# Kernel optimization log

Measured on AMD Instinct MI355X. Metric: run time of the kernel, lower is better.

## Reference

```python
import jax, jax.numpy as jnp
import numpy as np

N, IN_C, HID, OUT_C, DEPTH = 4096, 128, 256, 128, 3
KS = [2048, 1024, 512]  # ceil(0.5 * N_level)
E = 131072


def glorot(key, fan_in, fan_out):
    lim = np.sqrt(6.0 / (fan_in + fan_out))
    return jax.random.uniform(key, (fan_in, fan_out), jnp.float32, -lim, lim)


def build_adj(edge_index, n):
    # symmetric, self-loop-free adjacency with unit edge weights
    A = jnp.zeros((n, n), jnp.float32)
    A = A.at[edge_index[0], edge_index[1]].set(1.0)
    A = jnp.maximum(A, A.T)
    return A * (1.0 - jnp.eye(n, dtype=jnp.float32))


def gcn(x, A, W, b):
    # GCNConv(improved=True): A_hat = A + 2I, symmetric normalization
    n = A.shape[0]
    Ah = A + 2.0 * jnp.eye(n, dtype=A.dtype)
    deg = Ah.sum(axis=1)
    dinv = jnp.where(deg > 0, deg ** -0.5, 0.0)
    An = dinv[:, None] * Ah * dinv[None, :]
    return An @ (x @ W) + b


def augment(A):
    # remove self loops, add self loops (w=1), square (spspmm), remove self loops
    n = A.shape[0]
    I = jnp.eye(n, dtype=A.dtype)
    Al = A * (1.0 - I) + I
    A2 = Al @ Al
    return A2 * (1.0 - I)


def topk_pool(x, A, p, k):
    score = jnp.tanh((x @ p) / jnp.linalg.norm(p))
    vals, perm = jax.lax.top_k(score, k)
    return x[perm] * vals[:, None], A[perm][:, perm], perm


def setup_inputs() -> dict:
    key = jax.random.key(0)
    ks = jax.random.split(key, 16)
    x = jax.random.normal(ks[0], (N, IN_C), jnp.float32)
    edge_index = jax.random.randint(ks[1], (2, E), 0, N, jnp.int32)
    d = {"x": x, "edge_index": edge_index}
    d["Wd0"], d["bd0"] = glorot(ks[2], IN_C, HID), jnp.zeros((HID,), jnp.float32)
    d["Wd1"], d["bd1"] = glorot(ks[3], HID, HID), jnp.zeros((HID,), jnp.float32)
    d["Wd2"], d["bd2"] = glorot(ks[4], HID, HID), jnp.zeros((HID,), jnp.float32)
    d["Wd3"], d["bd3"] = glorot(ks[5], HID, HID), jnp.zeros((HID,), jnp.float32)
    d["p1"] = jax.random.normal(ks[6], (HID,), jnp.float32)
    d["p2"] = jax.random.normal(ks[7], (HID,), jnp.float32)
    d["p3"] = jax.random.normal(ks[8], (HID,), jnp.float32)
    d["Wu0"], d["bu0"] = glorot(ks[9], HID, HID), jnp.zeros((HID,), jnp.float32)
    d["Wu1"], d["bu1"] = glorot(ks[10], HID, HID), jnp.zeros((HID,), jnp.float32)
    d["Wu2"], d["bu2"] = glorot(ks[11], HID, OUT_C), jnp.zeros((OUT_C,), jnp.float32)
    return d


def reference(x, edge_index, Wd0, bd0, Wd1, bd1, Wd2, bd2, Wd3, bd3,
              p1, p2, p3, Wu0, bu0, Wu1, bu1, Wu2, bu2):
    n = x.shape[0]
    A = build_adj(edge_index, n)
    x = jax.nn.relu(gcn(x, A, Wd0, bd0))
    xs, As, perms = [x], [A], []
    down = [(Wd1, bd1), (Wd2, bd2), (Wd3, bd3)]
    pools = [p1, p2, p3]
    for i in range(DEPTH):
        A = augment(A)
        x, A, perm = topk_pool(x, A, pools[i], KS[i])
        x = jax.nn.relu(gcn(x, A, *down[i]))
        if i < DEPTH - 1:
            xs.append(x)
            As.append(A)
        perms.append(perm)
    up = [(Wu0, bu0), (Wu1, bu1), (Wu2, bu2)]
    for i in range(DEPTH):
        j = DEPTH - 1 - i
        res, perm = xs[j], perms[j]
        u = jnp.zeros_like(res).at[perm].set(x)
        x = res + u  # sum_res=True
        x = gcn(x, As[j], *up[i])
        if i < DEPTH - 1:
            x = jax.nn.relu(x)
    return x
```

## Files before the change

kernel.cpp:

```cpp
#include <hip/hip_runtime.h>


typedef __attribute__((ext_vector_type(8))) short bf16x8;
typedef __attribute__((ext_vector_type(4))) short s16x4;
typedef __attribute__((ext_vector_type(4))) float f32x4;

__device__ __forceinline__ short f2bf(float f) {
    unsigned u = __builtin_bit_cast(unsigned, f);
    u += 0x7FFFu + ((u >> 16) & 1u);
    return (short)(u >> 16);
}
__device__ __forceinline__ float bf2f(short s) {
    unsigned u = ((unsigned)(unsigned short)s) << 16;
    return __builtin_bit_cast(float, u);
}

#define GLL16(gsrc, ldst)                                                        \
    __builtin_amdgcn_global_load_lds(                                            \
        (__attribute__((address_space(1))) void*)(gsrc),                         \
        (__attribute__((address_space(3))) void*)(ldst), 16, 0, 0)

template<int MODE, int EPI>
__global__ __launch_bounds__(256, 2)
void gemm_bt(const short* __restrict__ Ah, const short* __restrict__ Al,
             const short* __restrict__ Bh, const short* __restrict__ Bl,
             float* __restrict__ Cf, int M, int N, int K, int kChunk)
{
    if (EPI == 1 && (int)blockIdx.y > (int)blockIdx.x) return;

    __shared__ short sAh[128 * 32];
    __shared__ short sBh[128 * 32];
    __shared__ short sAl[(MODE == 2) ? 128 * 32 : 8];
    __shared__ short sBl[(MODE >= 1) ? 128 * 32 : 8];

    const int t    = threadIdx.x;
    const int lane = t & 63;
    const int wave = t >> 6;
    const int tM   = blockIdx.y * 128;
    const int tN   = blockIdx.x * 128;
    const int k0   = blockIdx.z * kChunk;

    const int wm  = (wave >> 1) * 64;
    const int wn  = (wave & 1) * 64;
    const int l15 = lane & 15;
    const int g8  = (lane >> 4) * 8;

    f32x4 acc[4][4];
    const f32x4 zero = {0.f, 0.f, 0.f, 0.f};
#pragma unroll
    for (int i = 0; i < 4; i++)
#pragma unroll
        for (int j = 0; j < 4; j++) acc[i][j] = zero;

    const int i0 = t, i1 = t + 256;
    const short* a0 = Ah + (size_t)(tM + (i0 >> 2)) * K + (i0 & 3) * 8;
    const short* a1 = Ah + (size_t)(tM + (i1 >> 2)) * K + (i1 & 3) * 8;
    const short* b0 = Bh + (size_t)(tN + (i0 >> 2)) * K + (i0 & 3) * 8;
    const short* b1 = Bh + (size_t)(tN + (i1 >> 2)) * K + (i1 & 3) * 8;
    const short *bl0 = nullptr, *bl1 = nullptr, *al0 = nullptr, *al1 = nullptr;
    if (MODE >= 1) {
        bl0 = Bl + (size_t)(tN + (i0 >> 2)) * K + (i0 & 3) * 8;
        bl1 = Bl + (size_t)(tN + (i1 >> 2)) * K + (i1 & 3) * 8;
    }
    if (MODE == 2) {
        al0 = Al + (size_t)(tM + (i0 >> 2)) * K + (i0 & 3) * 8;
        al1 = Al + (size_t)(tM + (i1 >> 2)) * K + (i1 & 3) * 8;
    }

    for (int kb = k0; kb < k0 + kChunk; kb += 32) {
        GLL16(a0 + kb, &sAh[i0 * 8]);
        GLL16(a1 + kb, &sAh[i1 * 8]);
        GLL16(b0 + kb, &sBh[i0 * 8]);
        GLL16(b1 + kb, &sBh[i1 * 8]);
        if (MODE >= 1) { GLL16(bl0 + kb, &sBl[i0 * 8]); GLL16(bl1 + kb, &sBl[i1 * 8]); }
        if (MODE == 2) { GLL16(al0 + kb, &sAl[i0 * 8]); GLL16(al1 + kb, &sAl[i1 * 8]); }
        __syncthreads();

        bf16x8 aF[4], bF[4], aL[4], bL[4];
#pragma unroll
        for (int i = 0; i < 4; i++)
            aF[i] = *(const bf16x8*)&sAh[(wm + i * 16 + l15) * 32 + g8];
#pragma unroll
        for (int j = 0; j < 4; j++)
            bF[j] = *(const bf16x8*)&sBh[(wn + j * 16 + l15) * 32 + g8];
        if (MODE >= 1)
#pragma unroll
            for (int j = 0; j < 4; j++)
                bL[j] = *(const bf16x8*)&sBl[(wn + j * 16 + l15) * 32 + g8];
        if (MODE == 2)
#pragma unroll
            for (int i = 0; i < 4; i++)
                aL[i] = *(const bf16x8*)&sAl[(wm + i * 16 + l15) * 32 + g8];

#pragma unroll
        for (int i = 0; i < 4; i++)
#pragma unroll
            for (int j = 0; j < 4; j++) {
                acc[i][j] = __builtin_amdgcn_mfma_f32_16x16x32_bf16(aF[i], bF[j], acc[i][j], 0, 0, 0);
                if (MODE >= 1)
                    acc[i][j] = __builtin_amdgcn_mfma_f32_16x16x32_bf16(aF[i], bL[j], acc[i][j], 0, 0, 0);
                if (MODE == 2)
                    acc[i][j] = __builtin_amdgcn_mfma_f32_16x16x32_bf16(aL[i], bF[j], acc[i][j], 0, 0, 0);
            }
        __syncthreads();
    }

    const int r4 = (lane >> 4) * 4;
    if (EPI == 3) {
        float* CT = Cf + (size_t)blockIdx.z * M * N;
#pragma unroll
        for (int i = 0; i < 4; i++)
#pragma unroll
            for (int j = 0; j < 4; j++) {
                const int col   = tN + wn + j * 16 + l15;
                const int rbase = tM + wm + i * 16 + r4;
                *(f32x4*)&CT[(size_t)col * M + rbase] = acc[i][j];
            }
    } else {
        float* Cg = Cf + (size_t)blockIdx.z * M * N;
#pragma unroll
        for (int i = 0; i < 4; i++)
#pragma unroll
            for (int j = 0; j < 4; j++) {
                const int col = tN + wn + j * 16 + l15;
                float* cp = Cg + (size_t)(tM + wm + i * 16 + r4) * N + col;
#pragma unroll
                for (int r = 0; r < 4; r++) cp[(size_t)r * N] = acc[i][j][r];
            }
        if (EPI == 1 && tM != tN) {
#pragma unroll
            for (int i = 0; i < 4; i++)
#pragma unroll
                for (int j = 0; j < 4; j++) {
                    const int col   = tN + wn + j * 16 + l15;
                    const int rbase = tM + wm + i * 16 + r4;
                    *(f32x4*)&Cg[(size_t)col * N + rbase] = acc[i][j];
                }
        }
    }
}


__global__ void prep(const float* __restrict__ Wd0, const float* __restrict__ Wd1,
                     const float* __restrict__ Wd2, const float* __restrict__ Wd3,
                     const float* __restrict__ Wu0, const float* __restrict__ Wu1,
                     const float* __restrict__ Wu2, const float* __restrict__ x0,
                     short* __restrict__ Wth, short* __restrict__ Wtl,
                     short* __restrict__ Xh, short* __restrict__ Xl,
                     unsigned long long* __restrict__ M0)
{
    int t = blockIdx.x * 256 + threadIdx.x;
    float v; int dst;
    if (t < 32768)       { int e = t;          v = Wd0[e]; dst = 0      + (e & 255) * 128 + (e >> 8); }
    else if (t < 98304)  { int e = t - 32768;  v = Wd1[e]; dst = 32768  + (e & 255) * 256 + (e >> 8); }
    else if (t < 163840) { int e = t - 98304;  v = Wd2[e]; dst = 98304  + (e & 255) * 256 + (e >> 8); }
    else if (t < 229376) { int e = t - 163840; v = Wd3[e]; dst = 163840 + (e & 255) * 256 + (e >> 8); }
    else if (t < 294912) { int e = t - 229376; v = Wu0[e]; dst = 229376 + (e & 255) * 256 + (e >> 8); }
    else if (t < 360448) { int e = t - 294912; v = Wu1[e]; dst = 294912 + (e & 255) * 256 + (e >> 8); }
    else if (t < 393216) { int e = t - 360448; v = Wu2[e]; dst = 360448 + (e & 127) * 256 + (e >> 7); }
    else if (t < 917504) {
        int e = t - 393216;
        v = x0[e];
        short h = f2bf(v);
        Xh[e] = h; Xl[e] = f2bf(v - bf2f(h));
        return;
    } else {
        M0[t - 917504] = 0ull;
        return;
    }
    short h = f2bf(v);
    Wth[dst] = h; Wtl[dst] = f2bf(v - bf2f(h));
}

__global__ void build_bits(const int* __restrict__ ei, int E,
                           unsigned long long* __restrict__ M0)
{
    int e = blockIdx.x * 256 + threadIdx.x;
    if (e >= E) return;
    int i = ei[e], j = ei[E + e];
    if (i != j) {
        atomicOr(&M0[(size_t)i * 64 + (j >> 6)], 1ull << (j & 63));
        atomicOr(&M0[(size_t)j * 64 + (i >> 6)], 1ull << (i & 63));
    }
}

__global__ void row_compact_bits(const unsigned long long* __restrict__ M0,
                                 int* __restrict__ csr, float* __restrict__ rs)
{
    int row = blockIdx.x * 4 + (threadIdx.x >> 6);
    int lane = threadIdx.x & 63;
    unsigned long long w = M0[(size_t)row * 64 + lane];
    int c = __popcll(w);
    int incl = c;
    for (int off = 1; off < 64; off <<= 1) {
        int v = __shfl_up(incl, off);
        if (lane >= off) incl += v;
    }
    int base = incl - c;
    int* out = csr + (size_t)row * 128;
    while (w) {
        int b = __ffsll((unsigned long long)w) - 1;
        if (base < 128) out[base] = lane * 64 + b;
        base++;
        w &= w - 1;
    }
    if (lane == 63) rs[row] = (float)incl;
}

__global__ void mask_gather(const unsigned long long* __restrict__ M0,
                            const int* __restrict__ perm,
                            unsigned long long* __restrict__ mask,
                            float* __restrict__ rs, int kk)
{
    int t = blockIdx.x * 256 + threadIdx.x;
    if (t < kk) rs[t] = 0.f;
    int r = t >> 6, l = t & 63;
    int u = perm[r];
    unsigned long long w = M0[(size_t)u * 64 + l];
    if ((u >> 6) == l) w |= 1ull << (u & 63);
    mask[t] = w;
}

#define PSTR2 18
__global__ __launch_bounds__(256, 8)
void popc_aug_p(const unsigned long long* __restrict__ mask,
                short* __restrict__ Cp)
{
    const int bx = blockIdx.x, by = blockIdx.y, z = blockIdx.z;
    if (by > bx) return;
    __shared__ unsigned long long a[64 * PSTR2];
    __shared__ unsigned long long b[64 * PSTR2];
    const int t = threadIdx.x;
#pragma unroll
    for (int p = 0; p < 4; p++) {
        int idx = p * 256 + t;
        int rr = idx >> 4, w = idx & 15;
        a[rr * PSTR2 + w] = mask[((size_t)(by * 64 + rr)) * 64 + z * 16 + w];
        b[rr * PSTR2 + w] = mask[((size_t)(bx * 64 + rr)) * 64 + z * 16 + w];
    }
    __syncthreads();
    const int i0 = (t >> 4) * 4;
    const int j0 = t & 15;
    int acc[4][4];
#pragma unroll
    for (int qi = 0; qi < 4; qi++)
#pragma unroll
        for (int qj = 0; qj < 4; qj++) acc[qi][qj] = 0;
#pragma unroll
    for (int w = 0; w < 16; w += 2) {
        ulong2 av[4], bv[4];
#pragma unroll
        for (int q = 0; q < 4; q++) av[q] = *(const ulong2*)&a[(i0 + q) * PSTR2 + w];
#pragma unroll
        for (int q = 0; q < 4; q++) bv[q] = *(const ulong2*)&b[(j0 + 16 * q) * PSTR2 + w];
#pragma unroll
        for (int qi = 0; qi < 4; qi++)
#pragma unroll
            for (int qj = 0; qj < 4; qj++) {
                acc[qi][qj] += __builtin_popcountll(av[qi].x & bv[qj].x);
                acc[qi][qj] += __builtin_popcountll(av[qi].y & bv[qj].y);
            }
    }
    short* out = Cp + ((size_t)z * 1024 + (size_t)(by * 32 + bx)) * 4096;
#pragma unroll
    for (int qi = 0; qi < 4; qi++)
#pragma unroll
        for (int qj = 0; qj < 4; qj++)
            out[(i0 + qi) * 64 + j0 + 16 * qj] = (short)acc[qi][qj];
}

__global__ __launch_bounds__(256)
void aug_merge(const short* __restrict__ Cp, int kk,
               short* __restrict__ Ahs, float* __restrict__ rs)
{
    const int bx = blockIdx.x, by = blockIdx.y;
    if (by > bx) return;
    __shared__ float tile[64][65];
    __shared__ float rsum[64], csum[64];
    const int t = threadIdx.x;
    const int i  = t >> 2;
    const int c0 = (t & 3) * 16;
    const size_t tb = (size_t)(by * 32 + bx) * 4096;
    const size_t ss = (size_t)1024 * 4096;
    if (t < 64) { rsum[t] = 0.f; csum[t] = 0.f; }

    int v[16];
#pragma unroll
    for (int q = 0; q < 16; q++) v[q] = 0;
    for (int s = 0; s < 4; s++) {
        bf16x8 p0 = *(const bf16x8*)&Cp[tb + s * ss + i * 64 + c0];
        bf16x8 p1 = *(const bf16x8*)&Cp[tb + s * ss + i * 64 + c0 + 8];
#pragma unroll
        for (int q = 0; q < 8; q++) { v[q] += (int)p0[q]; v[8 + q] += (int)p1[q]; }
    }
    const int gi = by * 64 + i;
    float rp = 0.f;
    s16x4 pk[4];
#pragma unroll
    for (int q = 0; q < 16; q++) {
        const int gj = bx * 64 + c0 + q;
        float val = (gi == gj) ? 0.f : (float)v[q];
        tile[i][c0 + q] = val;
        rp += val;
        pk[q >> 2][q & 3] = f2bf(val);
    }
#pragma unroll
    for (int q = 0; q < 4; q++)
        *(s16x4*)&Ahs[(size_t)gi * kk + bx * 64 + c0 + q * 4] = pk[q];
    __syncthreads();
    atomicAdd(&rsum[i], rp);
    if (bx != by) {
        float cpv = 0.f;
#pragma unroll
        for (int q = 0; q < 16; q++) {
            float val = tile[c0 + q][i];
            cpv += val;
            pk[q >> 2][q & 3] = f2bf(val);
        }
#pragma unroll
        for (int q = 0; q < 4; q++)
            *(s16x4*)&Ahs[(size_t)(bx * 64 + i) * kk + by * 64 + c0 + q * 4] = pk[q];
        atomicAdd(&csum[i], cpv);
    }
    __syncthreads();
    if (t < 64) {
        atomicAdd(&rs[by * 64 + t], rsum[t]);
        if (bx != by) atomicAdd(&rs[bx * 64 + t], csum[t]);
    }
}

__global__ void z_reduce(const float* __restrict__ Cp, int S,
                         const float* __restrict__ rs,
                         short* __restrict__ Zh, short* __restrict__ Zl,
                         int n, int C)
{
    int t4 = (blockIdx.x * 256 + threadIdx.x) * 4;
    int r = t4 % n;
    size_t stride = (size_t)n * C;
    f32x4 v = {0.f, 0.f, 0.f, 0.f};
    for (int s = 0; s < S; s++) v += *(const f32x4*)&Cp[t4 + s * stride];
    f32x4 rsv = *(const f32x4*)&rs[r];
    s16x4 zh, zl;
#pragma unroll
    for (int q = 0; q < 4; q++) {
        float z = v[q] / sqrtf(rsv[q] + 2.f);
        short h = f2bf(z);
        zh[q] = h; zl[q] = f2bf(z - bf2f(h));
    }
    *(s16x4*)&Zh[t4] = zh;
    *(s16x4*)&Zl[t4] = zl;
}

__global__ void zf_reduce(const float* __restrict__ Cp, int S,
                          const float* __restrict__ rs,
                          float* __restrict__ Zf, int n, int C)
{
    int t4 = (blockIdx.x * 256 + threadIdx.x) * 4;
    int r = t4 / C;
    size_t stride = (size_t)n * C;
    f32x4 v = {0.f, 0.f, 0.f, 0.f};
    for (int s = 0; s < S; s++) v += *(const f32x4*)&Cp[t4 + s * stride];
    float d = 1.f / sqrtf(rs[r] + 2.f);
    v *= d;
    *(f32x4*)&Zf[t4] = v;
}

template<int CN, int RELU>
__global__ __launch_bounds__(256)
void spmm_gcn(const int* __restrict__ csr, const float* __restrict__ rs,
              const float* __restrict__ Zf, const float* __restrict__ b,
              float* __restrict__ out)
{
    const int lane = threadIdx.x & 63;
    const int row  = blockIdx.x * 4 + (threadIdx.x >> 6);
    const int dg   = (int)rs[row];
    const int* nb  = csr + (size_t)row * 128;
    if (CN == 256) {
        const int c = lane * 4;
        float4 acc = {0.f, 0.f, 0.f, 0.f};
        int q = 0;
        for (; q + 4 <= dg; q += 4) {
            int j0 = nb[q], j1 = nb[q+1], j2 = nb[q+2], j3 = nb[q+3];
            float4 z0 = *(const float4*)&Zf[(size_t)j0 * CN + c];
            float4 z1 = *(const float4*)&Zf[(size_t)j1 * CN + c];
            float4 z2 = *(const float4*)&Zf[(size_t)j2 * CN + c];
            float4 z3 = *(const float4*)&Zf[(size_t)j3 * CN + c];
            acc.x += z0.x; acc.y += z0.y; acc.z += z0.z; acc.w += z0.w;
            acc.x += z1.x; acc.y += z1.y; acc.z += z1.z; acc.w += z1.w;
            acc.x += z2.x; acc.y += z2.y; acc.z += z2.z; acc.w += z2.w;
            acc.x += z3.x; acc.y += z3.y; acc.z += z3.z; acc.w += z3.w;
        }
        for (; q < dg; q++) {
            float4 z = *(const float4*)&Zf[(size_t)nb[q] * CN + c];
            acc.x += z.x; acc.y += z.y; acc.z += z.z; acc.w += z.w;
        }
        float d = 1.f / sqrtf(rs[row] + 2.f);
        float4 zi = *(const float4*)&Zf[(size_t)row * CN + c];
        float4 bb = *(const float4*)&b[c];
        float4 g;
        g.x = d * acc.x + 2.f * d * zi.x + bb.x;
        g.y = d * acc.y + 2.f * d * zi.y + bb.y;
        g.z = d * acc.z + 2.f * d * zi.z + bb.z;
        g.w = d * acc.w + 2.f * d * zi.w + bb.w;
        if (RELU) {
            g.x = fmaxf(g.x, 0.f); g.y = fmaxf(g.y, 0.f);
            g.z = fmaxf(g.z, 0.f); g.w = fmaxf(g.w, 0.f);
        }
        *(float4*)&out[(size_t)row * CN + c] = g;
    } else {
        const int c = lane * 2;
        float2 acc = {0.f, 0.f};
        int q = 0;
        for (; q + 4 <= dg; q += 4) {
            int j0 = nb[q], j1 = nb[q+1], j2 = nb[q+2], j3 = nb[q+3];
            float2 z0 = *(const float2*)&Zf[(size_t)j0 * CN + c];
            float2 z1 = *(const float2*)&Zf[(size_t)j1 * CN + c];
            float2 z2 = *(const float2*)&Zf[(size_t)j2 * CN + c];
            float2 z3 = *(const float2*)&Zf[(size_t)j3 * CN + c];
            acc.x += z0.x; acc.y += z0.y;
            acc.x += z1.x; acc.y += z1.y;
            acc.x += z2.x; acc.y += z2.y;
            acc.x += z3.x; acc.y += z3.y;
        }
        for (; q < dg; q++) {
            float2 z = *(const float2*)&Zf[(size_t)nb[q] * CN + c];
            acc.x += z.x; acc.y += z.y;
        }
        float d = 1.f / sqrtf(rs[row] + 2.f);
        float2 zi = *(const float2*)&Zf[(size_t)row * CN + c];
        float2 g;
        g.x = d * acc.x + 2.f * d * zi.x + b[c];
        g.y = d * acc.y + 2.f * d * zi.y + b[c + 1];
        if (RELU) { g.x = fmaxf(g.x, 0.f); g.y = fmaxf(g.y, 0.f); }
        *(float2*)&out[(size_t)row * CN + c] = g;
    }
}

__global__ void gcn_final(const float* __restrict__ Cp, int S,
                          const short* __restrict__ Zh, const short* __restrict__ Zl,
                          const float* __restrict__ rs, const float* __restrict__ b,
                          float* __restrict__ out, short* __restrict__ oh,
                          short* __restrict__ ol, int k, int C, int relu,
                          const int* __restrict__ inv, const float* __restrict__ res)
{
    int t4 = (blockIdx.x * 256 + threadIdx.x) * 4;
    int j = t4 / C, c = t4 - j * C;
    int r = inv ? inv[j] : j;
    f32x4 v = res ? *(const f32x4*)&res[t4] : (f32x4){0.f, 0.f, 0.f, 0.f};
    if (r >= 0) {
        size_t base = (size_t)r * C + c;
        size_t stride = (size_t)k * C;
        f32x4 az = {0.f, 0.f, 0.f, 0.f};
        for (int s = 0; s < S; s++) az += *(const f32x4*)&Cp[base + s * stride];
        float d = 1.f / sqrtf(rs[r] + 2.f);
        f32x4 bb = *(const f32x4*)&b[c];
#pragma unroll
        for (int q = 0; q < 4; q++) {
            size_t zi = (size_t)(c + q) * k + r;
            float zz = bf2f(Zh[zi]) + bf2f(Zl[zi]);
            float g = d * az[q] + 2.f * d * zz + bb[q];
            if (relu && g < 0.f) g = 0.f;
            v[q] += g;
        }
    }
    *(f32x4*)&out[t4] = v;
    if (oh) {
        s16x4 hh, ll;
#pragma unroll
        for (int q = 0; q < 4; q++) {
            short h = f2bf(v[q]);
            hh[q] = h; ll[q] = f2bf(v[q] - bf2f(h));
        }
        *(s16x4*)&oh[t4] = hh;
        *(s16x4*)&ol[t4] = ll;
    }
}

__global__ void score_kernel(const float* __restrict__ x,
                             const float* __restrict__ p,
                             float* __restrict__ score, int n,
                             int* __restrict__ rankb)
{
    int row = blockIdx.x * 4 + (threadIdx.x >> 6);
    int lane = threadIdx.x & 63;
    float4 pv = ((const float4*)p)[lane];
    float4 xv = ((const float4*)(x + (size_t)row * 256))[lane];
    double nn  = (double)pv.x * pv.x + (double)pv.y * pv.y +
                 (double)pv.z * pv.z + (double)pv.w * pv.w;
    double acc = (double)xv.x * pv.x + (double)xv.y * pv.y +
                 (double)xv.z * pv.z + (double)xv.w * pv.w;
    for (int off = 32; off; off >>= 1) {
        acc += __shfl_down(acc, off);
        nn  += __shfl_down(nn, off);
    }
    if (lane == 0) {
        score[row] = tanhf((float)(acc / sqrt(nn)));
        rankb[row] = 0;
    }
}

__device__ __forceinline__ unsigned long long packkey(float s, int i) {
    unsigned u = __builtin_bit_cast(unsigned, s);
    u = (u & 0x80000000u) ? ~u : (u | 0x80000000u);
    return ((unsigned long long)u << 32) | (unsigned)(0xFFFFFFFFu - (unsigned)i);
}

__global__ __launch_bounds__(256)
void rank_count(const float* __restrict__ score,
                int* __restrict__ rankb)
{
    __shared__ unsigned long long sk[256];
    int i = blockIdx.x * 256 + threadIdx.x;
    int j = blockIdx.y * 256 + threadIdx.x;
    sk[threadIdx.x] = packkey(score[j], j);
    unsigned long long mykey = packkey(score[i], i);
    __syncthreads();
    int part = 0;
#pragma unroll 16
    for (int q = 0; q < 256; q++) part += (sk[q] > mykey) ? 1 : 0;
    atomicAdd(&rankb[i], part);
}

__global__ void rank_final(const float* __restrict__ score,
                           const int* __restrict__ rankb, int k,
                           int* __restrict__ perm, float* __restrict__ vals,
                           int* __restrict__ inv)
{
    int i = blockIdx.x * 256 + threadIdx.x;
    int rank = rankb[i];
    if (rank < k) { perm[rank] = i; vals[rank] = score[i]; }
    inv[i] = (rank < k) ? rank : -1;
}

__global__ void gather_x_hl(const float* __restrict__ xold,
                            const int* __restrict__ perm,
                            const float* __restrict__ vals,
                            short* __restrict__ Xh, short* __restrict__ Xl, int C)
{
    int t4 = (blockIdx.x * 256 + threadIdx.x) * 4;
    int r = t4 / C, c = t4 - r * C;
    float vv = vals[r];
    f32x4 x = *(const f32x4*)&xold[(size_t)perm[r] * C + c];
    s16x4 hh, ll;
#pragma unroll
    for (int q = 0; q < 4; q++) {
        float v = x[q] * vv;
        short h = f2bf(v);
        hh[q] = h; ll[q] = f2bf(v - bf2f(h));
    }
    *(s16x4*)&Xh[t4] = hh;
    *(s16x4*)&Xl[t4] = ll;
}

__global__ void gatherG_h(const short* __restrict__ A, int n,
                          const int* __restrict__ perm,
                          short* __restrict__ Gh, int kk,
                          float* __restrict__ rsz)
{
    int idx = blockIdx.x * 256 + threadIdx.x;
    if (idx < kk) rsz[idx] = 0.f;
    int t8 = idx * 8;
    if (t8 >= kk * n) return;
    int r = t8 / n, c0 = t8 - r * n;
    int pr = perm[r];
    bf16x8 a = *(const bf16x8*)&A[(size_t)pr * n + c0];
    if (pr >= c0 && pr < c0 + 8)
        a[pr - c0] = f2bf(bf2f(a[pr - c0]) + 1.f);
    *(bf16x8*)&Gh[t8] = a;
}

__global__ void gatherG_hl(const short* __restrict__ Ahi, const short* __restrict__ Alo,
                           int n, const int* __restrict__ perm,
                           short* __restrict__ Gh, short* __restrict__ Gl, int kk,
                           float* __restrict__ rsz)
{
    int idx = blockIdx.x * 256 + threadIdx.x;
    if (idx < kk) rsz[idx] = 0.f;
    int t8 = idx * 8;
    if (t8 >= kk * n) return;
    int r = t8 / n, c0 = t8 - r * n;
    int pr = perm[r];
    bf16x8 ah = *(const bf16x8*)&Ahi[(size_t)pr * n + c0];
    bf16x8 al = *(const bf16x8*)&Alo[(size_t)pr * n + c0];
    bf16x8 gh, gl;
#pragma unroll
    for (int q = 0; q < 8; q++) {
        float v = bf2f(ah[q]) + bf2f(al[q]) + ((c0 + q == pr) ? 1.f : 0.f);
        short h = f2bf(v);
        gh[q] = h; gl[q] = f2bf(v - bf2f(h));
    }
    *(bf16x8*)&Gh[t8] = gh;
    *(bf16x8*)&Gl[t8] = gl;
}

template<bool LO>
__global__ void aug_finish_f(const float* __restrict__ Cp, int S, int kk,
                             short* __restrict__ Ahs, short* __restrict__ Als,
                             float* __restrict__ rs)
{
    int t4 = (blockIdx.x * 256 + threadIdx.x) * 4;
    int r = t4 / kk, c0 = t4 - r * kk;
    size_t stride = (size_t)kk * kk;
    f32x4 v = {0.f, 0.f, 0.f, 0.f};
    for (int s = 0; s < S; s++) v += *(const f32x4*)&Cp[t4 + s * stride];
    if (r >= c0 && r < c0 + 4) v[r - c0] = 0.f;
    s16x4 hh, ll;
    float ws = 0.f;
#pragma unroll
    for (int q = 0; q < 4; q++) {
        short h = f2bf(v[q]);
        hh[q] = h;
        if (LO) ll[q] = f2bf(v[q] - bf2f(h));
        ws += v[q];
    }
    *(s16x4*)&Ahs[t4] = hh;
    if (LO) *(s16x4*)&Als[t4] = ll;
    for (int off = 32; off; off >>= 1) ws += __shfl_down(ws, off);
    if ((threadIdx.x & 63) == 0) atomicAdd(&rs[r], ws);
}


extern "C" void kernel_launch(void* const* d_in, const int* in_sizes, int n_in,
                              void* d_out, int out_size, void* d_ws, size_t ws_size,
                              hipStream_t stream)
{
    const float* x0  = (const float*)d_in[0];
    const int*   ei  = (const int*)d_in[1];
    const float* Wd0 = (const float*)d_in[2];  const float* bd0 = (const float*)d_in[3];
    const float* Wd1 = (const float*)d_in[4];  const float* bd1 = (const float*)d_in[5];
    const float* Wd2 = (const float*)d_in[6];  const float* bd2 = (const float*)d_in[7];
    const float* Wd3 = (const float*)d_in[8];  const float* bd3 = (const float*)d_in[9];
    const float* p1  = (const float*)d_in[10];
    const float* p2  = (const float*)d_in[11];
    const float* p3  = (const float*)d_in[12];
    const float* Wu0 = (const float*)d_in[13]; const float* bu0 = (const float*)d_in[14];
    const float* Wu1 = (const float*)d_in[15]; const float* bu1 = (const float*)d_in[16];
    const float* Wu2 = (const float*)d_in[17]; const float* bu2 = (const float*)d_in[18];

    const int E = in_sizes[1] / 2;

    char* ws = (char*)d_ws;
    size_t off = 0;
    auto alloc = [&](size_t bytes) -> void* {
        void* p = ws + off;
        off += (bytes + 255) & ~(size_t)255;
        return p;
    };
    unsigned long long* M0 = (unsigned long long*)alloc((size_t)4096 * 64 * 8);
    short* A1h  = (short*)alloc((size_t)2048 * 2048 * 2);
    short* A2h  = (short*)alloc((size_t)1024 * 1024 * 2);
    short* A2l  = (short*)alloc((size_t)1024 * 1024 * 2);
    short* A3h  = (short*)alloc((size_t)512 * 512 * 2);
    short* A3l  = (short*)alloc((size_t)512 * 512 * 2);
    short* Gh   = (short*)alloc((size_t)1024 * 2048 * 2);
    short* Gl   = (short*)alloc((size_t)512 * 1024 * 2);
    int*   csr  = (int*)alloc((size_t)4096 * 128 * 4);
    unsigned long long* maskb = (unsigned long long*)alloc((size_t)2048 * 64 * 8);
    float* Zf   = (float*)alloc((size_t)4096 * 256 * 4);
    float* Cp   = (float*)alloc((size_t)64 * 1024 * 1024);
    float* xs0  = (float*)alloc((size_t)4096 * 256 * 4);
    float* xs1  = (float*)alloc((size_t)2048 * 256 * 4);
    float* xs2  = (float*)alloc((size_t)1024 * 256 * 4);
    float* xu0  = (float*)alloc((size_t)4096 * 256 * 4);
    float* xu1  = (float*)alloc((size_t)2048 * 256 * 4);
    float* xu2  = (float*)alloc((size_t)1024 * 256 * 4);
    short* xu0h = (short*)alloc((size_t)4096 * 256 * 2);
    short* xu0l = (short*)alloc((size_t)4096 * 256 * 2);
    short* xu1h = (short*)alloc((size_t)2048 * 256 * 2);
    short* xu1l = (short*)alloc((size_t)2048 * 256 * 2);
    short* xu2h = (short*)alloc((size_t)1024 * 256 * 2);
    short* xu2l = (short*)alloc((size_t)1024 * 256 * 2);
    short* X0h  = (short*)alloc((size_t)4096 * 128 * 2);
    short* X0l  = (short*)alloc((size_t)4096 * 128 * 2);
    short* xah  = (short*)alloc((size_t)2048 * 256 * 2);
    short* xal  = (short*)alloc((size_t)2048 * 256 * 2);
    short* Wth  = (short*)alloc((size_t)393216 * 2);
    short* Wtl  = (short*)alloc((size_t)393216 * 2);
    short* Zh   = (short*)alloc((size_t)256 * 4096 * 2);
    short* Zl   = (short*)alloc((size_t)256 * 4096 * 2);
    float* rs0  = (float*)alloc(4096 * 4);
    float* rs1  = (float*)alloc(2048 * 4);
    float* rs2  = (float*)alloc(1024 * 4);
    float* rs3  = (float*)alloc(512 * 4);
    float* scoreb = (float*)alloc(4096 * 4);
    float* valsb  = (float*)alloc(2048 * 4);
    int*   rankb  = (int*)alloc(4096 * 4);
    int*   perm1  = (int*)alloc(2048 * 4);
    int*   perm2  = (int*)alloc(1024 * 4);
    int*   perm3  = (int*)alloc(512 * 4);
    int*   inv1   = (int*)alloc(4096 * 4);
    int*   inv2   = (int*)alloc(2048 * 4);
    int*   inv3   = (int*)alloc(1024 * 4);

    auto gcn_dense = [&](const short* Xh, const short* Xl, int n, int Kc, int Cout,
                         const short* pAh, const short* pAl, const float* rsA,
                         int wtoff, const float* b,
                         float* out, short* oh, short* ol, int relu, int modeA,
                         int Saz, const int* inv, const float* res, int nout) {
        int Sxw = 4;
        gemm_bt<2, 3><<<dim3(Cout / 128, n / 128, Sxw), 256, 0, stream>>>(
            Xh, Xl, Wth + wtoff, Wtl + wtoff, Cp, n, Cout, Kc, Kc / Sxw);
        z_reduce<<<(n * Cout) / 1024, 256, 0, stream>>>(Cp, Sxw, rsA, Zh, Zl, n, Cout);
        dim3 g(Cout / 128, n / 128, Saz);
        if (modeA == 1)
            gemm_bt<1, 0><<<g, 256, 0, stream>>>(pAh, nullptr, Zh, Zl, Cp, n, Cout, n, n / Saz);
        else
            gemm_bt<2, 0><<<g, 256, 0, stream>>>(pAh, pAl, Zh, Zl, Cp, n, Cout, n, n / Saz);
        gcn_final<<<(nout * Cout) / 1024, 256, 0, stream>>>(
            Cp, Saz, Zh, Zl, rsA, b, out, oh, ol, n, Cout, relu, inv, res);
    };

    auto pool = [&](const float* xlev, int n, const float* p, int* perm, int* inv) {
        int k = n / 2;
        score_kernel<<<n / 4, 256, 0, stream>>>(xlev, p, scoreb, n, rankb);
        rank_count<<<dim3(n / 256, n / 256), 256, 0, stream>>>(scoreb, rankb);
        rank_final<<<n / 256, 256, 0, stream>>>(scoreb, rankb, k, perm, valsb, inv);
        gather_x_hl<<<k / 4, 256, 0, stream>>>(xlev, perm, valsb, xah, xal, 256);
    };

    prep<<<4608, 256, 0, stream>>>(Wd0, Wd1, Wd2, Wd3, Wu0, Wu1, Wu2, x0,
                                   Wth, Wtl, X0h, X0l, M0);
    build_bits<<<(E + 255) / 256, 256, 0, stream>>>(ei, E, M0);
    row_compact_bits<<<1024, 256, 0, stream>>>(M0, csr, rs0);

    gemm_bt<2, 0><<<dim3(2, 32, 4), 256, 0, stream>>>(
        X0h, X0l, Wth, Wtl, Cp, 4096, 256, 128, 32);
    zf_reduce<<<1024, 256, 0, stream>>>(Cp, 4, rs0, Zf, 4096, 256);
    spmm_gcn<256, 1><<<1024, 256, 0, stream>>>(csr, rs0, Zf, bd0, xs0);

    pool(xs0, 4096, p1, perm1, inv1);
    mask_gather<<<512, 256, 0, stream>>>(M0, perm1, maskb, rs1, 2048);
    popc_aug_p<<<dim3(32, 32, 4), 256, 0, stream>>>(maskb, (short*)Cp);
    aug_merge<<<dim3(32, 32), 256, 0, stream>>>((const short*)Cp, 2048, A1h, rs1);
    gcn_dense(xah, xal, 2048, 256, 256, A1h, nullptr, rs1, 32768, bd1,
              xs1, nullptr, nullptr, 1, 1, 8, nullptr, nullptr, 2048);

    pool(xs1, 2048, p2, perm2, inv2);
    gatherG_h<<<(1024 * 2048 / 8) / 256, 256, 0, stream>>>(A1h, 2048, perm2, Gh, 1024, rs2);
    gemm_bt<0, 1><<<dim3(8, 8, 8), 256, 0, stream>>>(Gh, nullptr, Gh, nullptr, Cp, 1024, 1024, 2048, 256);
    aug_finish_f<true><<<(1024 * 1024 / 4) / 256, 256, 0, stream>>>(Cp, 8, 1024, A2h, A2l, rs2);
    gcn_dense(xah, xal, 1024, 256, 256, A2h, A2l, rs2, 98304, bd2,
              xs2, nullptr, nullptr, 1, 2, 8, nullptr, nullptr, 1024);

    pool(xs2, 1024, p3, perm3, inv3);
    gatherG_hl<<<(512 * 1024 / 8) / 256, 256, 0, stream>>>(A2h, A2l, 1024, perm3, Gh, Gl, 512, rs3);
    gemm_bt<2, 1><<<dim3(4, 4, 8), 256, 0, stream>>>(Gh, Gl, Gh, Gl, Cp, 512, 512, 1024, 128);
    aug_finish_f<true><<<(512 * 512 / 4) / 256, 256, 0, stream>>>(Cp, 8, 512, A3h, A3l, rs3);

    gcn_dense(xah, xal, 512, 256, 256, A3h, A3l, rs3, 163840, bd3,
              xu2, xu2h, xu2l, 1, 2, 8, inv3, xs2, 1024);

    gcn_dense(xu2h, xu2l, 1024, 256, 256, A2h, A2l, rs2, 229376, bu0,
              xu1, xu1h, xu1l, 1, 2, 8, inv2, xs1, 2048);

    gcn_dense(xu1h, xu1l, 2048, 256, 256, A1h, nullptr, rs1, 294912, bu1,
              xu0, xu0h, xu0l, 1, 1, 8, inv1, xs0, 4096);

    gemm_bt<2, 0><<<dim3(1, 32, 8), 256, 0, stream>>>(
        xu0h, xu0l, Wth + 360448, Wtl + 360448, Cp, 4096, 128, 256, 32);
    zf_reduce<<<512, 256, 0, stream>>>(Cp, 8, rs0, Zf, 4096, 128);
    spmm_gcn<128, 0><<<1024, 256, 0, stream>>>(csr, rs0, Zf, bu2, (float*)d_out);
}
```

Measured before the change: 443.9 us.

## Fuse degree scaling into X@W GEMM epilogue and merge top-k select with gather

```diff
diff --git a/kernel.cpp b/kernel.cpp
--- a/kernel.cpp
+++ b/kernel.cpp
@@ -24,7 +24,8 @@
 __global__ __launch_bounds__(256, 2)
 void gemm_bt(const short* __restrict__ Ah, const short* __restrict__ Al,
              const short* __restrict__ Bh, const short* __restrict__ Bl,
-             float* __restrict__ Cf, int M, int N, int K, int kChunk)
+             float* __restrict__ Cf, short* __restrict__ Eh, short* __restrict__ El,
+             const float* __restrict__ rs, int M, int N, int K, int kChunk)
 {
     if (EPI == 1 && (int)blockIdx.y > (int)blockIdx.x) return;
 
@@ -106,16 +107,48 @@
     }
 
     const int r4 = (lane >> 4) * 4;
-    if (EPI == 3) {
-        float* CT = Cf + (size_t)blockIdx.z * M * N;
-#pragma unroll
-        for (int i = 0; i < 4; i++)
+    if (EPI == 2) {
+#pragma unroll
+        for (int i = 0; i < 4; i++) {
+            const int rbase = tM + wm + i * 16 + r4;
+            float dd[4];
+#pragma unroll
+            for (int r = 0; r < 4; r++) dd[r] = 1.f / sqrtf(rs[rbase + r] + 2.f);
 #pragma unroll
             for (int j = 0; j < 4; j++) {
-                const int col   = tN + wn + j * 16 + l15;
-                const int rbase = tM + wm + i * 16 + r4;
-                *(f32x4*)&CT[(size_t)col * M + rbase] = acc[i][j];
+                const int c = tN + wn + j * 16 + l15;
+                unsigned short zh[4], zl[4];
+#pragma unroll
+                for (int r = 0; r < 4; r++) {
+                    float z = acc[i][j][r] * dd[r];
+                    short h = f2bf(z);
+                    zh[r] = (unsigned short)h;
+                    zl[r] = (unsigned short)f2bf(z - bf2f(h));
+                }
+                uint2 ph, pl;
+                ph.x = (unsigned)zh[0] | ((unsigned)zh[1] << 16);
+                ph.y = (unsigned)zh[2] | ((unsigned)zh[3] << 16);
+                pl.x = (unsigned)zl[0] | ((unsigned)zl[1] << 16);
+                pl.y = (unsigned)zl[2] | ((unsigned)zl[3] << 16);
+                *(uint2*)&Eh[(size_t)c * M + rbase] = ph;
+                *(uint2*)&El[(size_t)c * M + rbase] = pl;
             }
+        }
+    } else if (EPI == 5) {
+#pragma unroll
+        for (int i = 0; i < 4; i++) {
+            const int rbase = tM + wm + i * 16 + r4;
+            float dd[4];
+#pragma unroll
+            for (int r = 0; r < 4; r++) dd[r] = 1.f / sqrtf(rs[rbase + r] + 2.f);
+#pragma unroll
+            for (int j = 0; j < 4; j++) {
+                const int c = tN + wn + j * 16 + l15;
+#pragma unroll
+                for (int r = 0; r < 4; r++)
+                    Cf[(size_t)(rbase + r) * N + c] = acc[i][j][r] * dd[r];
+            }
+        }
     } else {
         float* Cg = Cf + (size_t)blockIdx.z * M * N;
 #pragma unroll
@@ -329,42 +362,6 @@
     }
 }
 
-__global__ void z_reduce(const float* __restrict__ Cp, int S,
-                         const float* __restrict__ rs,
-                         short* __restrict__ Zh, short* __restrict__ Zl,
-                         int n, int C)
-{
-    int t4 = (blockIdx.x * 256 + threadIdx.x) * 4;
-    int r = t4 % n;
-    size_t stride = (size_t)n * C;
-    f32x4 v = {0.f, 0.f, 0.f, 0.f};
-    for (int s = 0; s < S; s++) v += *(const f32x4*)&Cp[t4 + s * stride];
-    f32x4 rsv = *(const f32x4*)&rs[r];
-    s16x4 zh, zl;
-#pragma unroll
-    for (int q = 0; q < 4; q++) {
-        float z = v[q] / sqrtf(rsv[q] + 2.f);
-        short h = f2bf(z);
-        zh[q] = h; zl[q] = f2bf(z - bf2f(h));
-    }
-    *(s16x4*)&Zh[t4] = zh;
-    *(s16x4*)&Zl[t4] = zl;
-}
-
-__global__ void zf_reduce(const float* __restrict__ Cp, int S,
-                          const float* __restrict__ rs,
-                          float* __restrict__ Zf, int n, int C)
-{
-    int t4 = (blockIdx.x * 256 + threadIdx.x) * 4;
-    int r = t4 / C;
-    size_t stride = (size_t)n * C;
-    f32x4 v = {0.f, 0.f, 0.f, 0.f};
-    for (int s = 0; s < S; s++) v += *(const f32x4*)&Cp[t4 + s * stride];
-    float d = 1.f / sqrtf(rs[r] + 2.f);
-    v *= d;
-    *(f32x4*)&Zf[t4] = v;
-}
-
 template<int CN, int RELU>
 __global__ __launch_bounds__(256)
 void spmm_gcn(const int* __restrict__ csr, const float* __restrict__ rs,
@@ -521,35 +518,30 @@
     atomicAdd(&rankb[i], part);
 }
 
-__global__ void rank_final(const float* __restrict__ score,
-                           const int* __restrict__ rankb, int k,
-                           int* __restrict__ perm, float* __restrict__ vals,
-                           int* __restrict__ inv)
-{
-    int i = blockIdx.x * 256 + threadIdx.x;
-    int rank = rankb[i];
-    if (rank < k) { perm[rank] = i; vals[rank] = score[i]; }
-    inv[i] = (rank < k) ? rank : -1;
-}
-
-__global__ void gather_x_hl(const float* __restrict__ xold,
-                            const int* __restrict__ perm,
-                            const float* __restrict__ vals,
-                            short* __restrict__ Xh, short* __restrict__ Xl, int C)
-{
-    int t4 = (blockIdx.x * 256 + threadIdx.x) * 4;
-    int r = t4 / C, c = t4 - r * C;
-    float vv = vals[r];
-    f32x4 x = *(const f32x4*)&xold[(size_t)perm[r] * C + c];
+__global__ __launch_bounds__(256)
+void select_gather(const float* __restrict__ score, const int* __restrict__ rankb,
+                   int k, const float* __restrict__ x,
+                   int* __restrict__ perm, float* __restrict__ vals,
+                   int* __restrict__ inv,
+                   short* __restrict__ Xh, short* __restrict__ Xl)
+{
+    const int row = blockIdx.x * 4 + (threadIdx.x >> 6);
+    const int lane = threadIdx.x & 63;
+    const int rank = rankb[row];
+    if (lane == 0) inv[row] = (rank < k) ? rank : -1;
+    if (rank >= k) return;
+    const float s = score[row];
+    if (lane == 0) { perm[rank] = row; vals[rank] = s; }
+    f32x4 xv = *(const f32x4*)&x[(size_t)row * 256 + lane * 4];
     s16x4 hh, ll;
 #pragma unroll
     for (int q = 0; q < 4; q++) {
-        float v = x[q] * vv;
+        float v = xv[q] * s;
         short h = f2bf(v);
         hh[q] = h; ll[q] = f2bf(v - bf2f(h));
     }
-    *(s16x4*)&Xh[t4] = hh;
-    *(s16x4*)&Xl[t4] = ll;
+    *(s16x4*)&Xh[(size_t)rank * 256 + lane * 4] = hh;
+    *(s16x4*)&Xl[(size_t)rank * 256 + lane * 4] = ll;
 }
 
 __global__ void gatherG_h(const short* __restrict__ A, int n,
@@ -697,15 +689,13 @@
                          int wtoff, const float* b,
                          float* out, short* oh, short* ol, int relu, int modeA,
                          int Saz, const int* inv, const float* res, int nout) {
-        int Sxw = 4;
-        gemm_bt<2, 3><<<dim3(Cout / 128, n / 128, Sxw), 256, 0, stream>>>(
-            Xh, Xl, Wth + wtoff, Wtl + wtoff, Cp, n, Cout, Kc, Kc / Sxw);
-        z_reduce<<<(n * Cout) / 1024, 256, 0, stream>>>(Cp, Sxw, rsA, Zh, Zl, n, Cout);
+        gemm_bt<2, 2><<<dim3(Cout / 128, n / 128, 1), 256, 0, stream>>>(
+            Xh, Xl, Wth + wtoff, Wtl + wtoff, nullptr, Zh, Zl, rsA, n, Cout, Kc, Kc);
         dim3 g(Cout / 128, n / 128, Saz);
         if (modeA == 1)
-            gemm_bt<1, 0><<<g, 256, 0, stream>>>(pAh, nullptr, Zh, Zl, Cp, n, Cout, n, n / Saz);
+            gemm_bt<1, 0><<<g, 256, 0, stream>>>(pAh, nullptr, Zh, Zl, Cp, nullptr, nullptr, nullptr, n, Cout, n, n / Saz);
         else
-            gemm_bt<2, 0><<<g, 256, 0, stream>>>(pAh, pAl, Zh, Zl, Cp, n, Cout, n, n / Saz);
+            gemm_bt<2, 0><<<g, 256, 0, stream>>>(pAh, pAl, Zh, Zl, Cp, nullptr, nullptr, nullptr, n, Cout, n, n / Saz);
         gcn_final<<<(nout * Cout) / 1024, 256, 0, stream>>>(
             Cp, Saz, Zh, Zl, rsA, b, out, oh, ol, n, Cout, relu, inv, res);
     };
@@ -714,8 +704,8 @@
         int k = n / 2;
         score_kernel<<<n / 4, 256, 0, stream>>>(xlev, p, scoreb, n, rankb);
         rank_count<<<dim3(n / 256, n / 256), 256, 0, stream>>>(scoreb, rankb);
-        rank_final<<<n / 256, 256, 0, stream>>>(scoreb, rankb, k, perm, valsb, inv);
-        gather_x_hl<<<k / 4, 256, 0, stream>>>(xlev, perm, valsb, xah, xal, 256);
+        select_gather<<<n / 4, 256, 0, stream>>>(scoreb, rankb, k, xlev,
+                                                 perm, valsb, inv, xah, xal);
     };
 
     prep<<<4608, 256, 0, stream>>>(Wd0, Wd1, Wd2, Wd3, Wu0, Wu1, Wu2, x0,
@@ -723,9 +713,8 @@
     build_bits<<<(E + 255) / 256, 256, 0, stream>>>(ei, E, M0);
     row_compact_bits<<<1024, 256, 0, stream>>>(M0, csr, rs0);
 
-    gemm_bt<2, 0><<<dim3(2, 32, 4), 256, 0, stream>>>(
-        X0h, X0l, Wth, Wtl, Cp, 4096, 256, 128, 32);
-    zf_reduce<<<1024, 256, 0, stream>>>(Cp, 4, rs0, Zf, 4096, 256);
+    gemm_bt<2, 5><<<dim3(2, 32, 1), 256, 0, stream>>>(
+        X0h, X0l, Wth, Wtl, Zf, nullptr, nullptr, rs0, 4096, 256, 128, 128);
     spmm_gcn<256, 1><<<1024, 256, 0, stream>>>(csr, rs0, Zf, bd0, xs0);
 
     pool(xs0, 4096, p1, perm1, inv1);
@@ -737,14 +726,14 @@
 
     pool(xs1, 2048, p2, perm2, inv2);
     gatherG_h<<<(1024 * 2048 / 8) / 256, 256, 0, stream>>>(A1h, 2048, perm2, Gh, 1024, rs2);
-    gemm_bt<0, 1><<<dim3(8, 8, 8), 256, 0, stream>>>(Gh, nullptr, Gh, nullptr, Cp, 1024, 1024, 2048, 256);
+    gemm_bt<0, 1><<<dim3(8, 8, 8), 256, 0, stream>>>(Gh, nullptr, Gh, nullptr, Cp, nullptr, nullptr, nullptr, 1024, 1024, 2048, 256);
     aug_finish_f<true><<<(1024 * 1024 / 4) / 256, 256, 0, stream>>>(Cp, 8, 1024, A2h, A2l, rs2);
     gcn_dense(xah, xal, 1024, 256, 256, A2h, A2l, rs2, 98304, bd2,
               xs2, nullptr, nullptr, 1, 2, 8, nullptr, nullptr, 1024);
 
     pool(xs2, 1024, p3, perm3, inv3);
     gatherG_hl<<<(512 * 1024 / 8) / 256, 256, 0, stream>>>(A2h, A2l, 1024, perm3, Gh, Gl, 512, rs3);
-    gemm_bt<2, 1><<<dim3(4, 4, 8), 256, 0, stream>>>(Gh, Gl, Gh, Gl, Cp, 512, 512, 1024, 128);
+    gemm_bt<2, 1><<<dim3(4, 4, 8), 256, 0, stream>>>(Gh, Gl, Gh, Gl, Cp, nullptr, nullptr, nullptr, 512, 512, 1024, 128);
     aug_finish_f<true><<<(512 * 512 / 4) / 256, 256, 0, stream>>>(Cp, 8, 512, A3h, A3l, rs3);
 
     gcn_dense(xah, xal, 512, 256, 256, A3h, A3l, rs3, 163840, bd3,
@@ -756,8 +745,7 @@
     gcn_dense(xu1h, xu1l, 2048, 256, 256, A1h, nullptr, rs1, 294912, bu1,
               xu0, xu0h, xu0l, 1, 1, 8, inv1, xs0, 4096);
 
-    gemm_bt<2, 0><<<dim3(1, 32, 8), 256, 0, stream>>>(
-        xu0h, xu0l, Wth + 360448, Wtl + 360448, Cp, 4096, 128, 256, 32);
-    zf_reduce<<<512, 256, 0, stream>>>(Cp, 8, rs0, Zf, 4096, 128);
+    gemm_bt<2, 5><<<dim3(1, 32, 1), 256, 0, stream>>>(
+        xu0h, xu0l, Wth + 360448, Wtl + 360448, Zf, nullptr, nullptr, rs0, 4096, 128, 256, 256);
     spmm_gcn<128, 0><<<1024, 256, 0, stream>>>(csr, rs0, Zf, bu2, (float*)d_out);
 }
```

Measured after the change: 451.7 us. About the same (+1.8%).
